# Kernel optimization log

Hardware: AMD Instinct MI355X
Metric: run time of the kernel (lower is better)

The kernel has to match this reference:

```python
import jax, jax.numpy as jnp
import numpy as np
from jax import lax

VOCAB = 50257
EMB = 512
HID = 1024
SEQ = 4096
NUM_LAYERS = 2


def _lstm_layer(x_seq, h0, c0, w_ih, w_hh, b_ih, b_hh):
    """Single-layer LSTM over time. x_seq: [T, in], h0/c0: [H].
    PyTorch gate order: i, f, g, o."""
    # Precompute input projections for all timesteps: [T, 4H]
    xg = x_seq @ w_ih.T + (b_ih + b_hh)

    def step(carry, xg_t):
        h, c = carry
        g = xg_t + h @ w_hh.T  # [4H]
        i, f, gg, o = jnp.split(g, 4)
        i = jax.nn.sigmoid(i)
        f = jax.nn.sigmoid(f)
        gg = jnp.tanh(gg)
        o = jax.nn.sigmoid(o)
        c_new = f * c + i * gg
        h_new = o * jnp.tanh(c_new)
        return (h_new, c_new), h_new

    (h_n, c_n), hs = lax.scan(step, (h0, c0), xg)
    return hs, h_n, c_n  # hs: [T, H]


def setup_inputs() -> dict:
    key = jax.random.key(0)
    ks = jax.random.split(key, 12)
    s = 0.02
    inp = {
        "input": jax.random.randint(ks[0], (SEQ,), 0, VOCAB),
        "h0": jnp.zeros((NUM_LAYERS, 1, HID), jnp.float32),
        "c0": jnp.zeros((NUM_LAYERS, 1, HID), jnp.float32),
        "emb": jax.random.normal(ks[1], (VOCAB, EMB), jnp.float32) * s,
        "w_ih0": jax.random.normal(ks[2], (4 * HID, EMB), jnp.float32) * s,
        "w_hh0": jax.random.normal(ks[3], (4 * HID, HID), jnp.float32) * s,
        "b_ih0": jnp.zeros((4 * HID,), jnp.float32),
        "b_hh0": jnp.zeros((4 * HID,), jnp.float32),
        "w_ih1": jax.random.normal(ks[4], (4 * HID, HID), jnp.float32) * s,
        "w_hh1": jax.random.normal(ks[5], (4 * HID, HID), jnp.float32) * s,
        "b_ih1": jnp.zeros((4 * HID,), jnp.float32),
        "b_hh1": jnp.zeros((4 * HID,), jnp.float32),
        "w_out": jax.random.normal(ks[6], (VOCAB, HID), jnp.float32) * s,
        "b_out": jnp.zeros((VOCAB,), jnp.float32),
    }
    return inp


def reference(input, h0, c0, emb, w_ih0, w_hh0, b_ih0, b_hh0,
              w_ih1, w_hh1, b_ih1, b_hh1, w_out, b_out):
    # Embedding gather: [T, EMB] (batch dim of 1 is implicit)
    x = emb[input]
    # Layer 0
    hs0, h_n0, c_n0 = _lstm_layer(x, h0[0, 0], c0[0, 0], w_ih0, w_hh0, b_ih0, b_hh0)
    # Layer 1 consumes layer-0 hidden sequence
    hs1, h_n1, c_n1 = _lstm_layer(hs0, h0[1, 0], c0[1, 0], w_ih1, w_hh1, b_ih1, b_hh1)
    # lstm_out[-1]: [1, H]
    last = hs1[-1][None, :]
    logits = last @ w_out.T + b_out  # [1, VOCAB]
    output = jax.nn.log_softmax(logits, axis=1)
    h_n = jnp.stack([h_n0, h_n1])[:, None, :]  # [2, 1, H]
    c_n = jnp.stack([c_n0, c_n1])[:, None, :]
    return output, h_n, c_n
```

## Files before the change

### kernel.cpp

```cpp
#include <hip/hip_runtime.h>


#define T_SEQ 4096
#define HID   1024
#define EMBD  512
#define VOCAB 50257
#define NBLK  256
#define TPB   512
#define UB    4
#define NSEG0 48
#define NSEG1 64

#define WS_H0T 0
#define WS_H1T 2048
#define WS_H1F 4096
#define WS_LOG 5120
#define WS_LSE 55377

#define OFF_W0 0
#define OFF_W1 49152
#define OFF_V0 114688
#define OFF_V1 117760
#define OFF_GP 121856
#define OFF_B0 122304
#define OFF_B1 122368
#define SMEM_BYTES 122432

typedef __attribute__((ext_vector_type(8))) short short8;
typedef __attribute__((ext_vector_type(4))) float f32x4;
typedef unsigned long long u64;

__device__ __forceinline__ unsigned short f2bf(float f) {
  unsigned int u = __float_as_uint(f);
  u += 0x7FFFu + ((u >> 16) & 1u);
  return (unsigned short)(u >> 16);
}
__device__ __forceinline__ unsigned int pack2bf(float a, float b) {
  return (unsigned int)f2bf(a) | ((unsigned int)f2bf(b) << 16);
}
__device__ __forceinline__ float sigmoidf_(float x) {
  return 1.f / (1.f + __expf(-x));
}
__device__ __forceinline__ float tanhf_(float x) {
  return 1.f - 2.f / (__expf(2.f * x) + 1.f);
}

template<int CNT>
__device__ __forceinline__ void mm_part(const short8* vf, const short8* wf,
                                        int s0, int lane, float* gout) {
  f32x4 a0 = {0.f, 0.f, 0.f, 0.f};
  f32x4 a1 = a0, a2 = a0, a3 = a0;
  const int grp = lane >> 4;
#pragma unroll
  for (int i = 0; i < CNT; ++i) {
    const int seg = s0 + i;
    short8 av = vf[seg * 4 + grp];
    short8 bv = wf[seg * 64 + lane];
    if ((i & 3) == 0)      a0 = __builtin_amdgcn_mfma_f32_16x16x32_bf16(av, bv, a0, 0, 0, 0);
    else if ((i & 3) == 1) a1 = __builtin_amdgcn_mfma_f32_16x16x32_bf16(av, bv, a1, 0, 0, 0);
    else if ((i & 3) == 2) a2 = __builtin_amdgcn_mfma_f32_16x16x32_bf16(av, bv, a2, 0, 0, 0);
    else                   a3 = __builtin_amdgcn_mfma_f32_16x16x32_bf16(av, bv, a3, 0, 0, 0);
  }
  f32x4 s = (a0 + a1) + (a2 + a3);
  if (lane < 16) gout[lane] = s[0];
}

__global__ __launch_bounds__(TPB, 1) void reset_kernel(
    const float* __restrict__ h0in, unsigned int* __restrict__ ws) {
  const int tid = threadIdx.x;
  u64* H0T = reinterpret_cast<u64*>(ws + WS_H0T);
  u64* H1T = reinterpret_cast<u64*>(ws + WS_H1T);
  H0T[tid] = (u64)pack2bf(h0in[2 * tid], h0in[2 * tid + 1]);
  H1T[tid] = (u64)pack2bf(h0in[HID + 2 * tid], h0in[HID + 2 * tid + 1]);
}

__global__ __launch_bounds__(TPB, 1) void scan_kernel(
    const int* __restrict__ tok,
    const float* __restrict__ h0in, const float* __restrict__ c0in,
    const float* __restrict__ emb,
    const float* __restrict__ wih0, const float* __restrict__ whh0,
    const float* __restrict__ bih0, const float* __restrict__ bhh0,
    const float* __restrict__ wih1, const float* __restrict__ whh1,
    const float* __restrict__ bih1, const float* __restrict__ bhh1,
    float* __restrict__ dout, unsigned int* __restrict__ ws) {
  extern __shared__ char smem[];
  short8* W0f = reinterpret_cast<short8*>(smem + OFF_W0);
  short8* W1f = reinterpret_cast<short8*>(smem + OFF_W1);
  unsigned int* v0w = reinterpret_cast<unsigned int*>(smem + OFF_V0);
  unsigned int* v1w = reinterpret_cast<unsigned int*>(smem + OFF_V1);
  const short8* v0f = reinterpret_cast<const short8*>(smem + OFF_V0);
  const short8* v1f = reinterpret_cast<const short8*>(smem + OFF_V1);
  float* gp  = reinterpret_cast<float*>(smem + OFF_GP);
  float* bs0 = reinterpret_cast<float*>(smem + OFF_B0);
  float* bs1 = reinterpret_cast<float*>(smem + OFF_B1);

  const int tid = threadIdx.x;
  const int bid = blockIdx.x;
  const int lane = tid & 63;
  const int w = tid >> 6;

  for (int slot = tid; slot < NSEG0 * 64; slot += TPB) {
    const int seg = slot >> 6, l = slot & 63;
    const int col = l & 15, grp = l >> 4;
    const int grow = (col >> 2) * HID + bid * UB + (col & 3);
    const int k0 = seg * 32 + grp * 8;
    const float* src = (k0 < EMBD) ? (wih0 + (size_t)grow * EMBD + k0)
                                   : (whh0 + (size_t)grow * HID + (k0 - EMBD));
    const float4* s4 = reinterpret_cast<const float4*>(src);
    float4 f0 = s4[0], f1 = s4[1];
    short8 pk;
    pk[0] = (short)f2bf(f0.x); pk[1] = (short)f2bf(f0.y);
    pk[2] = (short)f2bf(f0.z); pk[3] = (short)f2bf(f0.w);
    pk[4] = (short)f2bf(f1.x); pk[5] = (short)f2bf(f1.y);
    pk[6] = (short)f2bf(f1.z); pk[7] = (short)f2bf(f1.w);
    W0f[slot] = pk;
  }
  for (int slot = tid; slot < NSEG1 * 64; slot += TPB) {
    const int seg = slot >> 6, l = slot & 63;
    const int col = l & 15, grp = l >> 4;
    const int grow = (col >> 2) * HID + bid * UB + (col & 3);
    const int k0 = seg * 32 + grp * 8;
    const float* src = (k0 < HID) ? (wih1 + (size_t)grow * HID + k0)
                                  : (whh1 + (size_t)grow * HID + (k0 - HID));
    const float4* s4 = reinterpret_cast<const float4*>(src);
    float4 f0 = s4[0], f1 = s4[1];
    short8 pk;
    pk[0] = (short)f2bf(f0.x); pk[1] = (short)f2bf(f0.y);
    pk[2] = (short)f2bf(f0.z); pk[3] = (short)f2bf(f0.w);
    pk[4] = (short)f2bf(f1.x); pk[5] = (short)f2bf(f1.y);
    pk[6] = (short)f2bf(f1.z); pk[7] = (short)f2bf(f1.w);
    W1f[slot] = pk;
  }
  if (tid < 16) {
    const int grow = (tid >> 2) * HID + bid * UB + (tid & 3);
    bs0[tid] = bih0[grow] + bhh0[grow];
  } else if (tid < 32) {
    const int c = tid - 16;
    const int grow = (c >> 2) * HID + bid * UB + (c & 3);
    bs1[c] = bih1[grow] + bhh1[grow];
  }

  float cst = 0.f;
  if (w == 0 && lane < UB) cst = c0in[bid * UB + lane];
  if (w == 3 && lane < UB) cst = c0in[HID + bid * UB + lane];

  float xa = 0.f, xb = 0.f;
  if (tid < 256) {
    const float* xp = emb + (size_t)tok[0] * EMBD + tid * 2;
    xa = xp[0]; xb = xp[1];
  }

  u64* H0T = reinterpret_cast<u64*>(ws + WS_H0T);
  u64* H1T = reinterpret_cast<u64*>(ws + WS_H1T);

  for (int r = 1; r <= T_SEQ + 1; ++r) {
    if (tid < 256) {
      v0w[tid] = pack2bf(xa, xb);
      const int ridx = (r < T_SEQ) ? r : (T_SEQ - 1);
      const float* xp = emb + (size_t)tok[ridx] * EMBD + tid * 2;
      xa = xp[0]; xb = xp[1];
    }

    {
      const int p0 = (r - 1) & 1;
      const int p1 = r & 1;
      const unsigned int tg0 = (unsigned int)(r - 1);
      const unsigned int tg1 = (unsigned int)(r - 2);
      const bool need1 = (r >= 2);
      u64 w0 = 0, w1 = 0;
      bool ok0 = false, ok1 = !need1;
      do {
        if (!ok0) {
          w0 = __hip_atomic_load(&H0T[p0 * 512 + tid], __ATOMIC_RELAXED,
                                 __HIP_MEMORY_SCOPE_AGENT);
          ok0 = ((unsigned int)(w0 >> 32) == tg0);
        }
        if (!ok1) {
          w1 = __hip_atomic_load(&H1T[p1 * 512 + tid], __ATOMIC_RELAXED,
                                 __HIP_MEMORY_SCOPE_AGENT);
          ok1 = ((unsigned int)(w1 >> 32) == tg1);
        }
      } while (!(ok0 && ok1));
      const unsigned int d0 = (unsigned int)w0;
      v0w[256 + tid] = d0;
      v1w[tid] = d0;
      if (need1) v1w[512 + tid] = (unsigned int)w1;
    }
    __syncthreads();

    if (w < 3) {
      if (r <= T_SEQ) mm_part<16>(v0f, W0f, w * 16, lane, gp + w * 16);
    } else if (w < 7) {
      if (r >= 2) mm_part<16>(v1f, W1f, (w - 3) * 16, lane, gp + w * 16);
    }
    __syncthreads();

    if (w == 0 && r <= T_SEQ) {
      float hv = 0.f;
      if (lane < UB) {
        const int u = lane;
        float gi = bs0[u], gf = bs0[4 + u], gg = bs0[8 + u], go = bs0[12 + u];
#pragma unroll
        for (int p = 0; p < 3; ++p) {
          gi += gp[p * 16 + u];      gf += gp[p * 16 + 4 + u];
          gg += gp[p * 16 + 8 + u];  go += gp[p * 16 + 12 + u];
        }
        const float c = sigmoidf_(gf) * cst + sigmoidf_(gi) * tanhf_(gg);
        cst = c;
        hv = sigmoidf_(go) * tanhf_(c);
        if (r == T_SEQ) {
          dout[VOCAB + bid * UB + u] = hv;
          dout[VOCAB + 2 * HID + bid * UB + u] = cst;
        }
      }
      const float a = __shfl(hv, 2 * (lane & 1));
      const float b = __shfl(hv, 2 * (lane & 1) + 1);
      if (lane < 2) {
        const u64 word = ((u64)(unsigned int)r << 32) | (u64)pack2bf(a, b);
        __hip_atomic_store(&H0T[(r & 1) * 512 + bid * 2 + lane], word,
                           __ATOMIC_RELAXED, __HIP_MEMORY_SCOPE_AGENT);
      }
    }
    if (w == 3 && r >= 2) {
      float hv = 0.f;
      if (lane < UB) {
        const int u = lane;
        float gi = bs1[u], gf = bs1[4 + u], gg = bs1[8 + u], go = bs1[12 + u];
#pragma unroll
        for (int p = 3; p < 7; ++p) {
          gi += gp[p * 16 + u];      gf += gp[p * 16 + 4 + u];
          gg += gp[p * 16 + 8 + u];  go += gp[p * 16 + 12 + u];
        }
        const float c = sigmoidf_(gf) * cst + sigmoidf_(gi) * tanhf_(gg);
        cst = c;
        hv = sigmoidf_(go) * tanhf_(c);
        if (r - 1 == T_SEQ) {
          float* h1f = reinterpret_cast<float*>(ws + WS_H1F);
          h1f[bid * UB + u] = hv;
          dout[VOCAB + HID + bid * UB + u] = hv;
          dout[VOCAB + 3 * HID + bid * UB + u] = cst;
        }
      }
      const float a = __shfl(hv, 2 * (lane & 1));
      const float b = __shfl(hv, 2 * (lane & 1) + 1);
      if (lane < 2) {
        const u64 word = ((u64)(unsigned int)(r - 1) << 32) | (u64)pack2bf(a, b);
        __hip_atomic_store(&H1T[((r - 1) & 1) * 512 + bid * 2 + lane], word,
                           __ATOMIC_RELAXED, __HIP_MEMORY_SCOPE_AGENT);
      }
    }
  }
}

__global__ __launch_bounds__(256) void logits_kernel(
    const float* __restrict__ wout, const float* __restrict__ bout,
    unsigned int* __restrict__ ws) {
  const float* h1f = reinterpret_cast<const float*>(ws + WS_H1F);
  float* lg = reinterpret_cast<float*>(ws + WS_LOG);
  const int lane = threadIdx.x & 63;
  const int wv = threadIdx.x >> 6;
  const int gw = blockIdx.x * 4 + wv;
  const float4* h4 = reinterpret_cast<const float4*>(h1f);
  float4 h[4];
#pragma unroll
  for (int j = 0; j < 4; ++j) h[j] = h4[j * 64 + lane];
  for (int v = gw; v < VOCAB; v += 1024) {
    const float4* wr = reinterpret_cast<const float4*>(wout + (size_t)v * HID);
    float s = 0.f;
#pragma unroll
    for (int j = 0; j < 4; ++j) {
      float4 x = wr[j * 64 + lane];
      s += x.x * h[j].x + x.y * h[j].y + x.z * h[j].z + x.w * h[j].w;
    }
#pragma unroll
    for (int m = 32; m >= 1; m >>= 1) s += __shfl_xor(s, m, 64);
    if (lane == 0) lg[v] = s + bout[v];
  }
}

__global__ __launch_bounds__(1024) void lse_kernel(unsigned int* __restrict__ ws) {
  const float* lg = reinterpret_cast<const float*>(ws + WS_LOG);
  __shared__ float wred[16];
  __shared__ float mshare;
  const int tid = threadIdx.x;
  float m = -3.4e38f;
  for (int i = tid; i < VOCAB; i += 1024) m = fmaxf(m, lg[i]);
#pragma unroll
  for (int s = 32; s >= 1; s >>= 1) m = fmaxf(m, __shfl_xor(m, s, 64));
  if ((tid & 63) == 0) wred[tid >> 6] = m;
  __syncthreads();
  if (tid == 0) {
    float mm = wred[0];
    for (int i = 1; i < 16; ++i) mm = fmaxf(mm, wred[i]);
    mshare = mm;
  }
  __syncthreads();
  const float M = mshare;
  float a = 0.f;
  for (int i = tid; i < VOCAB; i += 1024) a += __expf(lg[i] - M);
#pragma unroll
  for (int s = 32; s >= 1; s >>= 1) a += __shfl_xor(a, s, 64);
  __syncthreads();
  if ((tid & 63) == 0) wred[tid >> 6] = a;
  __syncthreads();
  if (tid == 0) {
    float ss = 0.f;
    for (int i = 0; i < 16; ++i) ss += wred[i];
    reinterpret_cast<float*>(ws + WS_LSE)[0] = M + logf(ss);
  }
}

__global__ __launch_bounds__(256) void out_kernel(
    const unsigned int* __restrict__ ws, float* __restrict__ dout) {
  const float lse = reinterpret_cast<const float*>(ws + WS_LSE)[0];
  const float* lg = reinterpret_cast<const float*>(ws + WS_LOG);
  const int i = blockIdx.x * 256 + threadIdx.x;
  if (i < VOCAB) dout[i] = lg[i] - lse;
}

extern "C" void kernel_launch(void* const* d_in, const int* in_sizes, int n_in,
                              void* d_out, int out_size, void* d_ws, size_t ws_size,
                              hipStream_t stream) {
  const int*   tok  = (const int*)d_in[0];
  const float* h0in = (const float*)d_in[1];
  const float* c0in = (const float*)d_in[2];
  const float* emb  = (const float*)d_in[3];
  const float* wih0 = (const float*)d_in[4];
  const float* whh0 = (const float*)d_in[5];
  const float* bih0 = (const float*)d_in[6];
  const float* bhh0 = (const float*)d_in[7];
  const float* wih1 = (const float*)d_in[8];
  const float* whh1 = (const float*)d_in[9];
  const float* bih1 = (const float*)d_in[10];
  const float* bhh1 = (const float*)d_in[11];
  const float* wout = (const float*)d_in[12];
  const float* bout = (const float*)d_in[13];
  float* out = (float*)d_out;
  unsigned int* ws = (unsigned int*)d_ws;

  (void)in_sizes; (void)n_in; (void)out_size; (void)ws_size;

  (void)hipFuncSetAttribute((const void*)scan_kernel,
                            hipFuncAttributeMaxDynamicSharedMemorySize, SMEM_BYTES);

  reset_kernel<<<1, TPB, 0, stream>>>(h0in, ws);
  scan_kernel<<<NBLK, TPB, SMEM_BYTES, stream>>>(
      tok, h0in, c0in, emb, wih0, whh0, bih0, bhh0,
      wih1, whh1, bih1, bhh1, out, ws);
  logits_kernel<<<256, 256, 0, stream>>>(wout, bout, ws);
  lse_kernel<<<1, 1024, 0, stream>>>(ws);
  out_kernel<<<(VOCAB + 255) / 256, 256, 0, stream>>>(ws, out);
}
```

Measured before the change: 12.72 ms.

## Cache weight fragments in registers and split hidden-state polling across half-blocks

Each wave now loads its 16 bf16 weight fragments from LDS into registers once before the time loop, so the per-step matmul only reads the activation vector from LDS. Hidden-state exchange switches from 8-byte relaxed atomics to 16-byte coherent (sc0 sc1) inline-asm loads and stores that each carry two tagged words. Threads 0-255 poll layer-0 state and threads 256-511 poll layer-1 state in parallel, instead of every thread polling both. The reset kernel also pre-tags the second buffer slot. The aim is to shorten the per-step sync and LDS latency on the serial critical path, at the cost of higher register pressure and reliance on hand-written cache-control asm and on 16-byte store atomicity.

```diff
diff --git a/kernel.cpp b/kernel.cpp
--- a/kernel.cpp
+++ b/kernel.cpp
@@ -28,6 +28,7 @@
 
 typedef __attribute__((ext_vector_type(8))) short short8;
 typedef __attribute__((ext_vector_type(4))) float f32x4;
+typedef __attribute__((ext_vector_type(4))) unsigned int u32x4;
 typedef unsigned long long u64;
 
 __device__ __forceinline__ unsigned short f2bf(float f) {
@@ -45,21 +46,28 @@
   return 1.f - 2.f / (__expf(2.f * x) + 1.f);
 }
 
-template<int CNT>
-__device__ __forceinline__ void mm_part(const short8* vf, const short8* wf,
-                                        int s0, int lane, float* gout) {
+__device__ __forceinline__ u32x4 load16_cohere(const void* p) {
+  u32x4 r;
+  asm volatile("global_load_dwordx4 %0, %1, off sc0 sc1\n\ts_waitcnt vmcnt(0)"
+               : "=v"(r) : "v"((u64)p) : "memory");
+  return r;
+}
+__device__ __forceinline__ void store16_cohere(void* p, u32x4 v) {
+  asm volatile("global_store_dwordx4 %0, %1, off sc0 sc1"
+               :: "v"((u64)p), "v"(v) : "memory");
+}
+
+__device__ __forceinline__ void mmv(const short8* vf, const short8 (&wr)[16],
+                                    int s0, int grp, float* gout, int lane) {
   f32x4 a0 = {0.f, 0.f, 0.f, 0.f};
   f32x4 a1 = a0, a2 = a0, a3 = a0;
-  const int grp = lane >> 4;
-#pragma unroll
-  for (int i = 0; i < CNT; ++i) {
-    const int seg = s0 + i;
-    short8 av = vf[seg * 4 + grp];
-    short8 bv = wf[seg * 64 + lane];
-    if ((i & 3) == 0)      a0 = __builtin_amdgcn_mfma_f32_16x16x32_bf16(av, bv, a0, 0, 0, 0);
-    else if ((i & 3) == 1) a1 = __builtin_amdgcn_mfma_f32_16x16x32_bf16(av, bv, a1, 0, 0, 0);
-    else if ((i & 3) == 2) a2 = __builtin_amdgcn_mfma_f32_16x16x32_bf16(av, bv, a2, 0, 0, 0);
-    else                   a3 = __builtin_amdgcn_mfma_f32_16x16x32_bf16(av, bv, a3, 0, 0, 0);
+#pragma unroll
+  for (int i = 0; i < 16; ++i) {
+    short8 av = vf[(s0 + i) * 4 + grp];
+    if ((i & 3) == 0)      a0 = __builtin_amdgcn_mfma_f32_16x16x32_bf16(av, wr[i], a0, 0, 0, 0);
+    else if ((i & 3) == 1) a1 = __builtin_amdgcn_mfma_f32_16x16x32_bf16(av, wr[i], a1, 0, 0, 0);
+    else if ((i & 3) == 2) a2 = __builtin_amdgcn_mfma_f32_16x16x32_bf16(av, wr[i], a2, 0, 0, 0);
+    else                   a3 = __builtin_amdgcn_mfma_f32_16x16x32_bf16(av, wr[i], a3, 0, 0, 0);
   }
   f32x4 s = (a0 + a1) + (a2 + a3);
   if (lane < 16) gout[lane] = s[0];
@@ -72,6 +80,8 @@
   u64* H1T = reinterpret_cast<u64*>(ws + WS_H1T);
   H0T[tid] = (u64)pack2bf(h0in[2 * tid], h0in[2 * tid + 1]);
   H1T[tid] = (u64)pack2bf(h0in[HID + 2 * tid], h0in[HID + 2 * tid + 1]);
+  H0T[512 + tid] = 0xFFFFFFFF00000000ULL;
+  H1T[512 + tid] = 0xFFFFFFFF00000000ULL;
 }
 
 __global__ __launch_bounds__(TPB, 1) void scan_kernel(
@@ -98,12 +108,13 @@
   const int bid = blockIdx.x;
   const int lane = tid & 63;
   const int w = tid >> 6;
+  const int grp = lane >> 4;
 
   for (int slot = tid; slot < NSEG0 * 64; slot += TPB) {
     const int seg = slot >> 6, l = slot & 63;
-    const int col = l & 15, grp = l >> 4;
+    const int col = l & 15, g = l >> 4;
     const int grow = (col >> 2) * HID + bid * UB + (col & 3);
-    const int k0 = seg * 32 + grp * 8;
+    const int k0 = seg * 32 + g * 8;
     const float* src = (k0 < EMBD) ? (wih0 + (size_t)grow * EMBD + k0)
                                    : (whh0 + (size_t)grow * HID + (k0 - EMBD));
     const float4* s4 = reinterpret_cast<const float4*>(src);
@@ -117,9 +128,9 @@
   }
   for (int slot = tid; slot < NSEG1 * 64; slot += TPB) {
     const int seg = slot >> 6, l = slot & 63;
-    const int col = l & 15, grp = l >> 4;
+    const int col = l & 15, g = l >> 4;
     const int grow = (col >> 2) * HID + bid * UB + (col & 3);
-    const int k0 = seg * 32 + grp * 8;
+    const int k0 = seg * 32 + g * 8;
     const float* src = (k0 < HID) ? (wih1 + (size_t)grow * HID + k0)
                                   : (whh1 + (size_t)grow * HID + (k0 - HID));
     const float4* s4 = reinterpret_cast<const float4*>(src);
@@ -139,6 +150,17 @@
     const int grow = (c >> 2) * HID + bid * UB + (c & 3);
     bs1[c] = bih1[grow] + bhh1[grow];
   }
+  __syncthreads();
+
+  short8 wr[16];
+  {
+    const short8* wf = (w < 3) ? W0f : W1f;
+    const int s0 = (w < 3) ? w * 16 : (w - 3) * 16;
+    if (w < 7) {
+#pragma unroll
+      for (int i = 0; i < 16; ++i) wr[i] = wf[(s0 + i) * 64 + lane];
+    }
+  }
 
   float cst = 0.f;
   if (w == 0 && lane < UB) cst = c0in[bid * UB + lane];
@@ -161,37 +183,28 @@
       xa = xp[0]; xb = xp[1];
     }
 
-    {
-      const int p0 = (r - 1) & 1;
-      const int p1 = r & 1;
+    if (tid < 256) {
       const unsigned int tg0 = (unsigned int)(r - 1);
+      const u64* src = &H0T[((r - 1) & 1) * 512 + 2 * tid];
+      u32x4 q;
+      do { q = load16_cohere(src); } while (q.y != tg0 || q.w != tg0);
+      const u64 pair = (u64)q.x | ((u64)q.z << 32);
+      *reinterpret_cast<u64*>(&v0w[256 + 2 * tid]) = pair;
+      *reinterpret_cast<u64*>(&v1w[2 * tid]) = pair;
+    } else if (r >= 2) {
+      const int t2 = tid - 256;
       const unsigned int tg1 = (unsigned int)(r - 2);
-      const bool need1 = (r >= 2);
-      u64 w0 = 0, w1 = 0;
-      bool ok0 = false, ok1 = !need1;
-      do {
-        if (!ok0) {
-          w0 = __hip_atomic_load(&H0T[p0 * 512 + tid], __ATOMIC_RELAXED,
-                                 __HIP_MEMORY_SCOPE_AGENT);
-          ok0 = ((unsigned int)(w0 >> 32) == tg0);
-        }
-        if (!ok1) {
-          w1 = __hip_atomic_load(&H1T[p1 * 512 + tid], __ATOMIC_RELAXED,
-                                 __HIP_MEMORY_SCOPE_AGENT);
-          ok1 = ((unsigned int)(w1 >> 32) == tg1);
-        }
-      } while (!(ok0 && ok1));
-      const unsigned int d0 = (unsigned int)w0;
-      v0w[256 + tid] = d0;
-      v1w[tid] = d0;
-      if (need1) v1w[512 + tid] = (unsigned int)w1;
+      const u64* src = &H1T[(r & 1) * 512 + 2 * t2];
+      u32x4 q;
+      do { q = load16_cohere(src); } while (q.y != tg1 || q.w != tg1);
+      *reinterpret_cast<u64*>(&v1w[512 + 2 * t2]) = (u64)q.x | ((u64)q.z << 32);
     }
     __syncthreads();
 
     if (w < 3) {
-      if (r <= T_SEQ) mm_part<16>(v0f, W0f, w * 16, lane, gp + w * 16);
+      if (r <= T_SEQ) mmv(v0f, wr, w * 16, grp, gp + w * 16, lane);
     } else if (w < 7) {
-      if (r >= 2) mm_part<16>(v1f, W1f, (w - 3) * 16, lane, gp + w * 16);
+      if (r >= 2) mmv(v1f, wr, (w - 3) * 16, grp, gp + w * 16, lane);
     }
     __syncthreads();
 
@@ -213,12 +226,13 @@
           dout[VOCAB + 2 * HID + bid * UB + u] = cst;
         }
       }
-      const float a = __shfl(hv, 2 * (lane & 1));
-      const float b = __shfl(hv, 2 * (lane & 1) + 1);
-      if (lane < 2) {
-        const u64 word = ((u64)(unsigned int)r << 32) | (u64)pack2bf(a, b);
-        __hip_atomic_store(&H0T[(r & 1) * 512 + bid * 2 + lane], word,
-                           __ATOMIC_RELAXED, __HIP_MEMORY_SCOPE_AGENT);
+      const float h0v = __shfl(hv, 0), h1v = __shfl(hv, 1);
+      const float h2v = __shfl(hv, 2), h3v = __shfl(hv, 3);
+      if (lane == 0) {
+        u32x4 word;
+        word.x = pack2bf(h0v, h1v); word.y = (unsigned int)r;
+        word.z = pack2bf(h2v, h3v); word.w = (unsigned int)r;
+        store16_cohere(&H0T[(r & 1) * 512 + bid * 2], word);
       }
     }
     if (w == 3 && r >= 2) {
@@ -241,12 +255,13 @@
           dout[VOCAB + 3 * HID + bid * UB + u] = cst;
         }
       }
-      const float a = __shfl(hv, 2 * (lane & 1));
-      const float b = __shfl(hv, 2 * (lane & 1) + 1);
-      if (lane < 2) {
-        const u64 word = ((u64)(unsigned int)(r - 1) << 32) | (u64)pack2bf(a, b);
-        __hip_atomic_store(&H1T[((r - 1) & 1) * 512 + bid * 2 + lane], word,
-                           __ATOMIC_RELAXED, __HIP_MEMORY_SCOPE_AGENT);
+      const float h0v = __shfl(hv, 0), h1v = __shfl(hv, 1);
+      const float h2v = __shfl(hv, 2), h3v = __shfl(hv, 3);
+      if (lane == 0) {
+        u32x4 word;
+        word.x = pack2bf(h0v, h1v); word.y = (unsigned int)(r - 1);
+        word.z = pack2bf(h2v, h3v); word.w = (unsigned int)(r - 1);
+        store16_cohere(&H1T[((r - 1) & 1) * 512 + bid * 2], word);
       }
     }
   }
```

Result: slower. 13.27 ms (+4.4%).

## Replace second block barrier with LDS flag handoff to a dedicated epilogue wave

Applied to the files above, without the earlier changes.

Removes the second __syncthreads per timestep. Each MFMA wave publishes a per-step LDS flag with release semantics, and a dedicated eighth wave spins on those flags with acquire loads before computing the LSTM cell updates for both layers. The input and hidden staging buffers are double-buffered by step parity so the next step's polling can overlap the epilogue. Polling of the global h words is also spread over 448 threads, each issuing three loads per spin. This cuts barrier latency on the serial recurrence path, at the cost of more LDS use, wave spinning, and subtle ordering risk around the buffer reuse.

```diff
diff --git a/kernel.cpp b/kernel.cpp
--- a/kernel.cpp
+++ b/kernel.cpp
@@ -7,6 +7,7 @@
 #define VOCAB 50257
 #define NBLK  256
 #define TPB   512
+#define NPOLL 448
 #define UB    4
 #define NSEG0 48
 #define NSEG1 64
@@ -20,11 +21,12 @@
 #define OFF_W0 0
 #define OFF_W1 49152
 #define OFF_V0 114688
-#define OFF_V1 117760
-#define OFF_GP 121856
-#define OFF_B0 122304
-#define OFF_B1 122368
-#define SMEM_BYTES 122432
+#define OFF_V1 120832
+#define OFF_GP 129024
+#define OFF_B0 129536
+#define OFF_B1 129600
+#define OFF_GF 129664
+#define SMEM_BYTES 129696
 
 typedef __attribute__((ext_vector_type(8))) short short8;
 typedef __attribute__((ext_vector_type(4))) float f32x4;
@@ -44,15 +46,16 @@
 __device__ __forceinline__ float tanhf_(float x) {
   return 1.f - 2.f / (__expf(2.f * x) + 1.f);
 }
-
-template<int CNT>
-__device__ __forceinline__ void mm_part(const short8* vf, const short8* wf,
-                                        int s0, int lane, float* gout) {
+__device__ __forceinline__ unsigned ldsacq(const unsigned* p) {
+  return __hip_atomic_load(p, __ATOMIC_ACQUIRE, __HIP_MEMORY_SCOPE_WORKGROUP);
+}
+
+__device__ __forceinline__ void mmv(const short8* vf, const short8* wf,
+                                    int s0, int grp, float* gout, int lane) {
   f32x4 a0 = {0.f, 0.f, 0.f, 0.f};
   f32x4 a1 = a0, a2 = a0, a3 = a0;
-  const int grp = lane >> 4;
-#pragma unroll
-  for (int i = 0; i < CNT; ++i) {
+#pragma unroll
+  for (int i = 0; i < 16; ++i) {
     const int seg = s0 + i;
     short8 av = vf[seg * 4 + grp];
     short8 bv = wf[seg * 64 + lane];
@@ -70,8 +73,12 @@
   const int tid = threadIdx.x;
   u64* H0T = reinterpret_cast<u64*>(ws + WS_H0T);
   u64* H1T = reinterpret_cast<u64*>(ws + WS_H1T);
-  H0T[tid] = (u64)pack2bf(h0in[2 * tid], h0in[2 * tid + 1]);
-  H1T[tid] = (u64)pack2bf(h0in[HID + 2 * tid], h0in[HID + 2 * tid + 1]);
+  const u64 w0 = (u64)pack2bf(h0in[2 * tid], h0in[2 * tid + 1]);
+  const u64 w1 = (u64)pack2bf(h0in[HID + 2 * tid], h0in[HID + 2 * tid + 1]);
+  __hip_atomic_store(&H0T[tid], w0, __ATOMIC_RELAXED, __HIP_MEMORY_SCOPE_AGENT);
+  __hip_atomic_store(&H1T[tid], w1, __ATOMIC_RELAXED, __HIP_MEMORY_SCOPE_AGENT);
+  __hip_atomic_store(&H0T[512 + tid], 0xFFFFFFFF00000000ULL, __ATOMIC_RELAXED, __HIP_MEMORY_SCOPE_AGENT);
+  __hip_atomic_store(&H1T[512 + tid], 0xFFFFFFFF00000000ULL, __ATOMIC_RELAXED, __HIP_MEMORY_SCOPE_AGENT);
 }
 
 __global__ __launch_bounds__(TPB, 1) void scan_kernel(
@@ -93,17 +100,19 @@
   float* gp  = reinterpret_cast<float*>(smem + OFF_GP);
   float* bs0 = reinterpret_cast<float*>(smem + OFF_B0);
   float* bs1 = reinterpret_cast<float*>(smem + OFF_B1);
+  unsigned* gpflag = reinterpret_cast<unsigned*>(smem + OFF_GF);
 
   const int tid = threadIdx.x;
   const int bid = blockIdx.x;
   const int lane = tid & 63;
   const int w = tid >> 6;
+  const int grp = lane >> 4;
 
   for (int slot = tid; slot < NSEG0 * 64; slot += TPB) {
     const int seg = slot >> 6, l = slot & 63;
-    const int col = l & 15, grp = l >> 4;
+    const int col = l & 15, g = l >> 4;
     const int grow = (col >> 2) * HID + bid * UB + (col & 3);
-    const int k0 = seg * 32 + grp * 8;
+    const int k0 = seg * 32 + g * 8;
     const float* src = (k0 < EMBD) ? (wih0 + (size_t)grow * EMBD + k0)
                                    : (whh0 + (size_t)grow * HID + (k0 - EMBD));
     const float4* s4 = reinterpret_cast<const float4*>(src);
@@ -117,9 +126,9 @@
   }
   for (int slot = tid; slot < NSEG1 * 64; slot += TPB) {
     const int seg = slot >> 6, l = slot & 63;
-    const int col = l & 15, grp = l >> 4;
+    const int col = l & 15, g = l >> 4;
     const int grow = (col >> 2) * HID + bid * UB + (col & 3);
-    const int k0 = seg * 32 + grp * 8;
+    const int k0 = seg * 32 + g * 8;
     const float* src = (k0 < HID) ? (wih1 + (size_t)grow * HID + k0)
                                   : (whh1 + (size_t)grow * HID + (k0 - HID));
     const float4* s4 = reinterpret_cast<const float4*>(src);
@@ -139,10 +148,13 @@
     const int grow = (c >> 2) * HID + bid * UB + (c & 3);
     bs1[c] = bih1[grow] + bhh1[grow];
   }
+  if (tid < 8) gpflag[tid] = 0u;
 
   float cst = 0.f;
-  if (w == 0 && lane < UB) cst = c0in[bid * UB + lane];
-  if (w == 3 && lane < UB) cst = c0in[HID + bid * UB + lane];
+  if (w == 7) {
+    if (lane < UB) cst = c0in[bid * UB + lane];
+    else if (lane >= 8 && lane < 8 + UB) cst = c0in[HID + bid * UB + (lane - 8)];
+  }
 
   float xa = 0.f, xb = 0.f;
   if (tid < 256) {
@@ -153,100 +165,138 @@
   u64* H0T = reinterpret_cast<u64*>(ws + WS_H0T);
   u64* H1T = reinterpret_cast<u64*>(ws + WS_H1T);
 
+  __syncthreads();
+
   for (int r = 1; r <= T_SEQ + 1; ++r) {
-    if (tid < 256) {
-      v0w[tid] = pack2bf(xa, xb);
-      const int ridx = (r < T_SEQ) ? r : (T_SEQ - 1);
-      const float* xp = emb + (size_t)tok[ridx] * EMBD + tid * 2;
-      xa = xp[0]; xb = xp[1];
-    }
-
-    {
+    const int pb = r & 1;
+
+    if (tid < NPOLL) {
+      if (tid < 256) {
+        v0w[pb * 768 + tid] = pack2bf(xa, xb);
+        const int ridx = (r < T_SEQ) ? r : (T_SEQ - 1);
+        const float* xp = emb + (size_t)tok[ridx] * EMBD + tid * 2;
+        xa = xp[0]; xb = xp[1];
+      }
+
       const int p0 = (r - 1) & 1;
       const int p1 = r & 1;
-      const unsigned int tg0 = (unsigned int)(r - 1);
-      const unsigned int tg1 = (unsigned int)(r - 2);
-      const bool need1 = (r >= 2);
-      u64 w0 = 0, w1 = 0;
-      bool ok0 = false, ok1 = !need1;
+      const unsigned tgh0 = (unsigned)(r - 1);
+      const unsigned tgh1 = (unsigned)(r - 2);
+      const int i0 = tid;
+      const int i1 = tid + 448;
+      const int i2 = (tid < 128) ? tid + 896 : tid;
+
+      u64* ap0 = &H0T[p0 * 512 + i0]; unsigned tg0 = tgh0;
+      u64 *ap1, *ap2; unsigned tg1, tg2;
+      if (i1 < 512)      { ap1 = &H0T[p0 * 512 + i1]; tg1 = tgh0; }
+      else if (r >= 2)   { ap1 = &H1T[p1 * 512 + (i1 - 512)]; tg1 = tgh1; }
+      else               { ap1 = ap0; tg1 = tg0; }
+      if (i2 < 512)      { ap2 = &H0T[p0 * 512 + i2]; tg2 = tgh0; }
+      else if (r >= 2)   { ap2 = &H1T[p1 * 512 + (i2 - 512)]; tg2 = tgh1; }
+      else               { ap2 = ap0; tg2 = tg0; }
+
+      u64 d0 = 0, d1 = 0, d2 = 0;
+      bool k0 = false, k1 = false, k2 = false;
       do {
-        if (!ok0) {
-          w0 = __hip_atomic_load(&H0T[p0 * 512 + tid], __ATOMIC_RELAXED,
-                                 __HIP_MEMORY_SCOPE_AGENT);
-          ok0 = ((unsigned int)(w0 >> 32) == tg0);
-        }
-        if (!ok1) {
-          w1 = __hip_atomic_load(&H1T[p1 * 512 + tid], __ATOMIC_RELAXED,
-                                 __HIP_MEMORY_SCOPE_AGENT);
-          ok1 = ((unsigned int)(w1 >> 32) == tg1);
-        }
-      } while (!(ok0 && ok1));
-      const unsigned int d0 = (unsigned int)w0;
-      v0w[256 + tid] = d0;
-      v1w[tid] = d0;
-      if (need1) v1w[512 + tid] = (unsigned int)w1;
+        const u64 s0 = __hip_atomic_load(ap0, __ATOMIC_RELAXED, __HIP_MEMORY_SCOPE_AGENT);
+        const u64 s1 = __hip_atomic_load(ap1, __ATOMIC_RELAXED, __HIP_MEMORY_SCOPE_AGENT);
+        const u64 s2 = __hip_atomic_load(ap2, __ATOMIC_RELAXED, __HIP_MEMORY_SCOPE_AGENT);
+        if (!k0 && (unsigned)(s0 >> 32) == tg0) { d0 = s0; k0 = true; }
+        if (!k1 && (unsigned)(s1 >> 32) == tg1) { d1 = s1; k1 = true; }
+        if (!k2 && (unsigned)(s2 >> 32) == tg2) { d2 = s2; k2 = true; }
+      } while (!(k0 && k1 && k2));
+
+      {
+        const unsigned lo = (unsigned)d0;
+        v0w[pb * 768 + 256 + i0] = lo;
+        v1w[pb * 1024 + i0] = lo;
+      }
+      if (i1 < 512) {
+        const unsigned lo = (unsigned)d1;
+        v0w[pb * 768 + 256 + i1] = lo;
+        v1w[pb * 1024 + i1] = lo;
+      } else if (r >= 2) {
+        v1w[pb * 1024 + 512 + (i1 - 512)] = (unsigned)d1;
+      }
+      if (tid < 128 && r >= 2) {
+        v1w[pb * 1024 + 512 + (i2 - 512)] = (unsigned)d2;
+      }
     }
     __syncthreads();
 
     if (w < 3) {
-      if (r <= T_SEQ) mm_part<16>(v0f, W0f, w * 16, lane, gp + w * 16);
+      if (r <= T_SEQ) {
+        mmv(v0f + pb * 192, W0f, w * 16, grp, gp + w * 16, lane);
+        if (lane == 0)
+          __hip_atomic_store(&gpflag[w], (unsigned)r, __ATOMIC_RELEASE,
+                             __HIP_MEMORY_SCOPE_WORKGROUP);
+      }
     } else if (w < 7) {
-      if (r >= 2) mm_part<16>(v1f, W1f, (w - 3) * 16, lane, gp + w * 16);
-    }
-    __syncthreads();
-
-    if (w == 0 && r <= T_SEQ) {
-      float hv = 0.f;
-      if (lane < UB) {
-        const int u = lane;
-        float gi = bs0[u], gf = bs0[4 + u], gg = bs0[8 + u], go = bs0[12 + u];
-#pragma unroll
-        for (int p = 0; p < 3; ++p) {
-          gi += gp[p * 16 + u];      gf += gp[p * 16 + 4 + u];
-          gg += gp[p * 16 + 8 + u];  go += gp[p * 16 + 12 + u];
+      if (r >= 2) {
+        mmv(v1f + pb * 256, W1f, (w - 3) * 16, grp, gp + w * 16, lane);
+        if (lane == 0)
+          __hip_atomic_store(&gpflag[w], (unsigned)r, __ATOMIC_RELEASE,
+                             __HIP_MEMORY_SCOPE_WORKGROUP);
+      }
+    } else {
+      const unsigned ru = (unsigned)r;
+      if (r <= T_SEQ) {
+        while (ldsacq(&gpflag[0]) < ru || ldsacq(&gpflag[1]) < ru ||
+               ldsacq(&gpflag[2]) < ru) { }
+        float hv = 0.f;
+        if (lane < UB) {
+          const int u = lane;
+          float gi = bs0[u], gf = bs0[4 + u], gg = bs0[8 + u], go = bs0[12 + u];
+#pragma unroll
+          for (int p = 0; p < 3; ++p) {
+            gi += gp[p * 16 + u];      gf += gp[p * 16 + 4 + u];
+            gg += gp[p * 16 + 8 + u];  go += gp[p * 16 + 12 + u];
+          }
+          const float c = sigmoidf_(gf) * cst + sigmoidf_(gi) * tanhf_(gg);
+          cst = c;
+          hv = sigmoidf_(go) * tanhf_(c);
+          if (r == T_SEQ) {
+            dout[VOCAB + bid * UB + u] = hv;
+            dout[VOCAB + 2 * HID + bid * UB + u] = cst;
+          }
         }
-        const float c = sigmoidf_(gf) * cst + sigmoidf_(gi) * tanhf_(gg);
-        cst = c;
-        hv = sigmoidf_(go) * tanhf_(c);
-        if (r == T_SEQ) {
-          dout[VOCAB + bid * UB + u] = hv;
-          dout[VOCAB + 2 * HID + bid * UB + u] = cst;
+        const float a = __shfl(hv, 2 * (lane & 1));
+        const float b = __shfl(hv, 2 * (lane & 1) + 1);
+        if (lane < 2) {
+          const u64 word = ((u64)ru << 32) | (u64)pack2bf(a, b);
+          __hip_atomic_store(&H0T[(r & 1) * 512 + bid * 2 + lane], word,
+                             __ATOMIC_RELAXED, __HIP_MEMORY_SCOPE_AGENT);
         }
       }
-      const float a = __shfl(hv, 2 * (lane & 1));
-      const float b = __shfl(hv, 2 * (lane & 1) + 1);
-      if (lane < 2) {
-        const u64 word = ((u64)(unsigned int)r << 32) | (u64)pack2bf(a, b);
-        __hip_atomic_store(&H0T[(r & 1) * 512 + bid * 2 + lane], word,
-                           __ATOMIC_RELAXED, __HIP_MEMORY_SCOPE_AGENT);
-      }
-    }
-    if (w == 3 && r >= 2) {
-      float hv = 0.f;
-      if (lane < UB) {
-        const int u = lane;
-        float gi = bs1[u], gf = bs1[4 + u], gg = bs1[8 + u], go = bs1[12 + u];
-#pragma unroll
-        for (int p = 3; p < 7; ++p) {
-          gi += gp[p * 16 + u];      gf += gp[p * 16 + 4 + u];
-          gg += gp[p * 16 + 8 + u];  go += gp[p * 16 + 12 + u];
+      if (r >= 2) {
+        while (ldsacq(&gpflag[3]) < ru || ldsacq(&gpflag[4]) < ru ||
+               ldsacq(&gpflag[5]) < ru || ldsacq(&gpflag[6]) < ru) { }
+        float hv = 0.f;
+        if (lane >= 8 && lane < 8 + UB) {
+          const int u = lane - 8;
+          float gi = bs1[u], gf = bs1[4 + u], gg = bs1[8 + u], go = bs1[12 + u];
+#pragma unroll
+          for (int p = 3; p < 7; ++p) {
+            gi += gp[p * 16 + u];      gf += gp[p * 16 + 4 + u];
+            gg += gp[p * 16 + 8 + u];  go += gp[p * 16 + 12 + u];
+          }
+          const float c = sigmoidf_(gf) * cst + sigmoidf_(gi) * tanhf_(gg);
+          cst = c;
+          hv = sigmoidf_(go) * tanhf_(c);
+          if (r - 1 == T_SEQ) {
+            float* h1f = reinterpret_cast<float*>(ws + WS_H1F);
+            h1f[bid * UB + u] = hv;
+            dout[VOCAB + HID + bid * UB + u] = hv;
+            dout[VOCAB + 3 * HID + bid * UB + u] = cst;
+          }
         }
-        const float c = sigmoidf_(gf) * cst + sigmoidf_(gi) * tanhf_(gg);
-        cst = c;
-        hv = sigmoidf_(go) * tanhf_(c);
-        if (r - 1 == T_SEQ) {
-          float* h1f = reinterpret_cast<float*>(ws + WS_H1F);
-          h1f[bid * UB + u] = hv;
-          dout[VOCAB + HID + bid * UB + u] = hv;
-          dout[VOCAB + 3 * HID + bid * UB + u] = cst;
+        const float a = __shfl(hv, 8 + 2 * (lane & 1));
+        const float b = __shfl(hv, 9 + 2 * (lane & 1));
+        if (lane >= 8 && lane < 10) {
+          const u64 word = ((u64)(unsigned)(r - 1) << 32) | (u64)pack2bf(a, b);
+          __hip_atomic_store(&H1T[((r - 1) & 1) * 512 + bid * 2 + (lane - 8)], word,
+                             __ATOMIC_RELAXED, __HIP_MEMORY_SCOPE_AGENT);
         }
-      }
-      const float a = __shfl(hv, 2 * (lane & 1));
-      const float b = __shfl(hv, 2 * (lane & 1) + 1);
-      if (lane < 2) {
-        const u64 word = ((u64)(unsigned int)(r - 1) << 32) | (u64)pack2bf(a, b);
-        __hip_atomic_store(&H1T[((r - 1) & 1) * 512 + bid * 2 + lane], word,
-                           __ATOMIC_RELAXED, __HIP_MEMORY_SCOPE_AGENT);
       }
     }
   }
```

Measured after the change: 19.97 ms. +57.0%, slower.

## Warp-specialize LSTM scan with register-resident weights and LDS flag sync

Applied to the files above, without the earlier changes.

Replaces the block-wide __syncthreads step loop with specialized wavefronts: loader waves poll the global hidden-state tags and fill double-buffered LDS vectors, while compute waves keep their bf16 weight slices in VGPRs and run MFMA. Coordination uses per-wave acquire/release flags in LDS. The point is to drop the two barriers per timestep, overlap the layer-0 and layer-1 polling with compute, and avoid re-reading weights from LDS every step. The cost is much more register pressure (up to 32 f32x4 weight fragments per lane), spin-wait LDS traffic, and a more fragile ordering protocol. The reset kernel also poisons the second parity buffer so stale tags cannot match.

```diff
diff --git a/kernel.cpp b/kernel.cpp
--- a/kernel.cpp
+++ b/kernel.cpp
@@ -8,8 +8,6 @@
 #define NBLK  256
 #define TPB   512
 #define UB    4
-#define NSEG0 48
-#define NSEG1 64
 
 #define WS_H0T 0
 #define WS_H1T 2048
@@ -20,11 +18,22 @@
 #define OFF_W0 0
 #define OFF_W1 49152
 #define OFF_V0 114688
-#define OFF_V1 117760
-#define OFF_GP 121856
-#define OFF_B0 122304
-#define OFF_B1 122368
-#define SMEM_BYTES 122432
+#define OFF_V1 120832
+#define OFF_PP0 124928
+#define OFF_PP1 125056
+#define OFF_B0 125184
+#define OFF_B1 125248
+#define OFF_FL 125312
+#define SMEM_BYTES 125376
+
+#define FL_SF0 0
+#define FL_SF1 1
+#define FL_SF4 4
+#define FL_SF5 5
+#define FL_PA0 8
+#define FL_PA1 9
+#define FL_C3  10
+#define FL_C7  11
 
 typedef __attribute__((ext_vector_type(8))) short short8;
 typedef __attribute__((ext_vector_type(4))) float f32x4;
@@ -44,25 +53,34 @@
 __device__ __forceinline__ float tanhf_(float x) {
   return 1.f - 2.f / (__expf(2.f * x) + 1.f);
 }
-
-template<int CNT>
-__device__ __forceinline__ void mm_part(const short8* vf, const short8* wf,
-                                        int s0, int lane, float* gout) {
+__device__ __forceinline__ unsigned ldsacq(const unsigned* p) {
+  return __hip_atomic_load(p, __ATOMIC_ACQUIRE, __HIP_MEMORY_SCOPE_WORKGROUP);
+}
+__device__ __forceinline__ void ldsrel(unsigned* p, unsigned v) {
+  __hip_atomic_store(p, v, __ATOMIC_RELEASE, __HIP_MEMORY_SCOPE_WORKGROUP);
+}
+__device__ __forceinline__ u64 agld(const u64* p) {
+  return __hip_atomic_load(p, __ATOMIC_RELAXED, __HIP_MEMORY_SCOPE_AGENT);
+}
+__device__ __forceinline__ void agst(u64* p, u64 v) {
+  __hip_atomic_store(p, v, __ATOMIC_RELAXED, __HIP_MEMORY_SCOPE_AGENT);
+}
+
+template<int NS>
+__device__ __forceinline__ f32x4 mm_regs(const f32x4 (&fr)[NS],
+                                         const short8* avb, int grp) {
   f32x4 a0 = {0.f, 0.f, 0.f, 0.f};
   f32x4 a1 = a0, a2 = a0, a3 = a0;
-  const int grp = lane >> 4;
-#pragma unroll
-  for (int i = 0; i < CNT; ++i) {
-    const int seg = s0 + i;
-    short8 av = vf[seg * 4 + grp];
-    short8 bv = wf[seg * 64 + lane];
+#pragma unroll
+  for (int i = 0; i < NS; ++i) {
+    short8 av = avb[i * 4 + grp];
+    short8 bv = __builtin_bit_cast(short8, fr[i]);
     if ((i & 3) == 0)      a0 = __builtin_amdgcn_mfma_f32_16x16x32_bf16(av, bv, a0, 0, 0, 0);
     else if ((i & 3) == 1) a1 = __builtin_amdgcn_mfma_f32_16x16x32_bf16(av, bv, a1, 0, 0, 0);
     else if ((i & 3) == 2) a2 = __builtin_amdgcn_mfma_f32_16x16x32_bf16(av, bv, a2, 0, 0, 0);
     else                   a3 = __builtin_amdgcn_mfma_f32_16x16x32_bf16(av, bv, a3, 0, 0, 0);
   }
-  f32x4 s = (a0 + a1) + (a2 + a3);
-  if (lane < 16) gout[lane] = s[0];
+  return (a0 + a1) + (a2 + a3);
 }
 
 __global__ __launch_bounds__(TPB, 1) void reset_kernel(
@@ -70,8 +88,12 @@
   const int tid = threadIdx.x;
   u64* H0T = reinterpret_cast<u64*>(ws + WS_H0T);
   u64* H1T = reinterpret_cast<u64*>(ws + WS_H1T);
-  H0T[tid] = (u64)pack2bf(h0in[2 * tid], h0in[2 * tid + 1]);
-  H1T[tid] = (u64)pack2bf(h0in[HID + 2 * tid], h0in[HID + 2 * tid + 1]);
+  const u64 w0 = (u64)pack2bf(h0in[2 * tid], h0in[2 * tid + 1]);
+  const u64 w1 = (u64)pack2bf(h0in[HID + 2 * tid], h0in[HID + 2 * tid + 1]);
+  agst(&H0T[tid], w0);
+  agst(&H1T[tid], w1);
+  agst(&H0T[512 + tid], 0xFFFFFFFF00000000ULL);
+  agst(&H1T[512 + tid], 0xFFFFFFFF00000000ULL);
 }
 
 __global__ __launch_bounds__(TPB, 1) void scan_kernel(
@@ -90,20 +112,23 @@
   unsigned int* v1w = reinterpret_cast<unsigned int*>(smem + OFF_V1);
   const short8* v0f = reinterpret_cast<const short8*>(smem + OFF_V0);
   const short8* v1f = reinterpret_cast<const short8*>(smem + OFF_V1);
-  float* gp  = reinterpret_cast<float*>(smem + OFF_GP);
+  float* pp0 = reinterpret_cast<float*>(smem + OFF_PP0);
+  float* pp1 = reinterpret_cast<float*>(smem + OFF_PP1);
   float* bs0 = reinterpret_cast<float*>(smem + OFF_B0);
   float* bs1 = reinterpret_cast<float*>(smem + OFF_B1);
+  unsigned* flg = reinterpret_cast<unsigned*>(smem + OFF_FL);
 
   const int tid = threadIdx.x;
   const int bid = blockIdx.x;
   const int lane = tid & 63;
   const int w = tid >> 6;
-
-  for (int slot = tid; slot < NSEG0 * 64; slot += TPB) {
+  const int grp = lane >> 4;
+
+  for (int slot = tid; slot < 48 * 64; slot += TPB) {
     const int seg = slot >> 6, l = slot & 63;
-    const int col = l & 15, grp = l >> 4;
+    const int col = l & 15, g = l >> 4;
     const int grow = (col >> 2) * HID + bid * UB + (col & 3);
-    const int k0 = seg * 32 + grp * 8;
+    const int k0 = seg * 32 + g * 8;
     const float* src = (k0 < EMBD) ? (wih0 + (size_t)grow * EMBD + k0)
                                    : (whh0 + (size_t)grow * HID + (k0 - EMBD));
     const float4* s4 = reinterpret_cast<const float4*>(src);
@@ -115,11 +140,11 @@
     pk[6] = (short)f2bf(f1.z); pk[7] = (short)f2bf(f1.w);
     W0f[slot] = pk;
   }
-  for (int slot = tid; slot < NSEG1 * 64; slot += TPB) {
+  for (int slot = tid; slot < 64 * 64; slot += TPB) {
     const int seg = slot >> 6, l = slot & 63;
-    const int col = l & 15, grp = l >> 4;
+    const int col = l & 15, g = l >> 4;
     const int grow = (col >> 2) * HID + bid * UB + (col & 3);
-    const int k0 = seg * 32 + grp * 8;
+    const int k0 = seg * 32 + g * 8;
     const float* src = (k0 < HID) ? (wih1 + (size_t)grow * HID + k0)
                                   : (whh1 + (size_t)grow * HID + (k0 - HID));
     const float4* s4 = reinterpret_cast<const float4*>(src);
@@ -139,115 +164,168 @@
     const int grow = (c >> 2) * HID + bid * UB + (c & 3);
     bs1[c] = bih1[grow] + bhh1[grow];
   }
-
-  float cst = 0.f;
-  if (w == 0 && lane < UB) cst = c0in[bid * UB + lane];
-  if (w == 3 && lane < UB) cst = c0in[HID + bid * UB + lane];
-
-  float xa = 0.f, xb = 0.f;
-  if (tid < 256) {
-    const float* xp = emb + (size_t)tok[0] * EMBD + tid * 2;
-    xa = xp[0]; xb = xp[1];
-  }
+  if (tid < 16) flg[tid] = 0u;
 
   u64* H0T = reinterpret_cast<u64*>(ws + WS_H0T);
   u64* H1T = reinterpret_cast<u64*>(ws + WS_H1T);
 
-  for (int r = 1; r <= T_SEQ + 1; ++r) {
-    if (tid < 256) {
-      v0w[tid] = pack2bf(xa, xb);
+  __syncthreads();
+
+  if (w < 2) {
+    const int t = tid;
+    const float4* emb4 = reinterpret_cast<const float4*>(emb);
+    float4 xcur = emb4[(size_t)tok[0] * 128 + t];
+    for (int r = 1; r <= T_SEQ + 1; ++r) {
+      const int p = r & 1;
       const int ridx = (r < T_SEQ) ? r : (T_SEQ - 1);
-      const float* xp = emb + (size_t)tok[ridx] * EMBD + tid * 2;
-      xa = xp[0]; xb = xp[1];
-    }
-
-    {
-      const int p0 = (r - 1) & 1;
-      const int p1 = r & 1;
-      const unsigned int tg0 = (unsigned int)(r - 1);
-      const unsigned int tg1 = (unsigned int)(r - 2);
-      const bool need1 = (r >= 2);
-      u64 w0 = 0, w1 = 0;
-      bool ok0 = false, ok1 = !need1;
+      float4 xnext = emb4[(size_t)tok[ridx] * 128 + t];
+      if (r >= 3) {
+        const unsigned need = (unsigned)(r - 2);
+        while (ldsacq(&flg[FL_C3]) < need || ldsacq(&flg[FL_PA1]) < need ||
+               ldsacq(&flg[FL_C7]) < need) { }
+      }
+      v0w[p * 768 + 2 * t]     = pack2bf(xcur.x, xcur.y);
+      v0w[p * 768 + 2 * t + 1] = pack2bf(xcur.z, xcur.w);
+      const unsigned tg = (unsigned)(r - 1);
+      u64* ap = &H0T[((r - 1) & 1) * 512 + 4 * t];
+      u64 d0 = 0, d1 = 0, d2 = 0, d3 = 0;
+      bool k0 = false, k1 = false, k2 = false, k3 = false;
       do {
-        if (!ok0) {
-          w0 = __hip_atomic_load(&H0T[p0 * 512 + tid], __ATOMIC_RELAXED,
-                                 __HIP_MEMORY_SCOPE_AGENT);
-          ok0 = ((unsigned int)(w0 >> 32) == tg0);
-        }
-        if (!ok1) {
-          w1 = __hip_atomic_load(&H1T[p1 * 512 + tid], __ATOMIC_RELAXED,
-                                 __HIP_MEMORY_SCOPE_AGENT);
-          ok1 = ((unsigned int)(w1 >> 32) == tg1);
-        }
-      } while (!(ok0 && ok1));
-      const unsigned int d0 = (unsigned int)w0;
-      v0w[256 + tid] = d0;
-      v1w[tid] = d0;
-      if (need1) v1w[512 + tid] = (unsigned int)w1;
-    }
-    __syncthreads();
-
-    if (w < 3) {
-      if (r <= T_SEQ) mm_part<16>(v0f, W0f, w * 16, lane, gp + w * 16);
-    } else if (w < 7) {
-      if (r >= 2) mm_part<16>(v1f, W1f, (w - 3) * 16, lane, gp + w * 16);
-    }
-    __syncthreads();
-
-    if (w == 0 && r <= T_SEQ) {
+        if (!k0) { d0 = agld(ap + 0); k0 = ((unsigned)(d0 >> 32) == tg); }
+        if (!k1) { d1 = agld(ap + 1); k1 = ((unsigned)(d1 >> 32) == tg); }
+        if (!k2) { d2 = agld(ap + 2); k2 = ((unsigned)(d2 >> 32) == tg); }
+        if (!k3) { d3 = agld(ap + 3); k3 = ((unsigned)(d3 >> 32) == tg); }
+      } while (!(k0 && k1 && k2 && k3));
+      unsigned* dst = &v0w[p * 768 + 256 + 4 * t];
+      dst[0] = (unsigned)d0; dst[1] = (unsigned)d1;
+      dst[2] = (unsigned)d2; dst[3] = (unsigned)d3;
+      ldsrel(&flg[w], (unsigned)r);
+      xcur = xnext;
+    }
+  } else if (w == 2) {
+    f32x4 fr[24];
+    const f32x4* Wr = reinterpret_cast<const f32x4*>(W0f);
+#pragma unroll
+    for (int i = 0; i < 24; ++i) fr[i] = Wr[i * 64 + lane];
+#pragma unroll
+    for (int i = 0; i < 24; ++i) asm volatile("" : "+v"(fr[i]));
+    for (int r = 1; r <= T_SEQ; ++r) {
+      const int p = r & 1;
+      const unsigned ru = (unsigned)r;
+      while (ldsacq(&flg[FL_SF0]) < ru || ldsacq(&flg[FL_SF1]) < ru) { }
+      f32x4 s = mm_regs<24>(fr, v0f + p * 192, grp);
+      if (lane < 16) pp0[p * 16 + lane] = s[0];
+      ldsrel(&flg[FL_PA0], ru);
+    }
+  } else if (w == 3) {
+    f32x4 fr[24];
+    const f32x4* Wr = reinterpret_cast<const f32x4*>(W0f);
+#pragma unroll
+    for (int i = 0; i < 24; ++i) fr[i] = Wr[(24 + i) * 64 + lane];
+#pragma unroll
+    for (int i = 0; i < 24; ++i) asm volatile("" : "+v"(fr[i]));
+    float cst = (lane < UB) ? c0in[bid * UB + lane] : 0.f;
+    for (int r = 1; r <= T_SEQ; ++r) {
+      const int p = r & 1;
+      const unsigned ru = (unsigned)r;
+      while (ldsacq(&flg[FL_SF0]) < ru || ldsacq(&flg[FL_SF1]) < ru) { }
+      f32x4 s = mm_regs<24>(fr, v0f + p * 192 + 96, grp);
+      ldsrel(&flg[FL_C3], ru);
+      while (ldsacq(&flg[FL_PA0]) < ru) { }
+      float g = 0.f;
+      if (lane < 16) g = s[0] + pp0[p * 16 + lane] + bs0[lane];
+      const int u = lane & 3;
+      const float gi = __shfl(g, u),      gf = __shfl(g, 4 + u);
+      const float gg = __shfl(g, 8 + u),  go = __shfl(g, 12 + u);
       float hv = 0.f;
       if (lane < UB) {
-        const int u = lane;
-        float gi = bs0[u], gf = bs0[4 + u], gg = bs0[8 + u], go = bs0[12 + u];
-#pragma unroll
-        for (int p = 0; p < 3; ++p) {
-          gi += gp[p * 16 + u];      gf += gp[p * 16 + 4 + u];
-          gg += gp[p * 16 + 8 + u];  go += gp[p * 16 + 12 + u];
-        }
         const float c = sigmoidf_(gf) * cst + sigmoidf_(gi) * tanhf_(gg);
         cst = c;
         hv = sigmoidf_(go) * tanhf_(c);
         if (r == T_SEQ) {
-          dout[VOCAB + bid * UB + u] = hv;
-          dout[VOCAB + 2 * HID + bid * UB + u] = cst;
+          dout[VOCAB + bid * UB + lane] = hv;
+          dout[VOCAB + 2 * HID + bid * UB + lane] = c;
         }
       }
       const float a = __shfl(hv, 2 * (lane & 1));
       const float b = __shfl(hv, 2 * (lane & 1) + 1);
-      if (lane < 2) {
-        const u64 word = ((u64)(unsigned int)r << 32) | (u64)pack2bf(a, b);
-        __hip_atomic_store(&H0T[(r & 1) * 512 + bid * 2 + lane], word,
-                           __ATOMIC_RELAXED, __HIP_MEMORY_SCOPE_AGENT);
-      }
-    }
-    if (w == 3 && r >= 2) {
+      if (lane < 2)
+        agst(&H0T[(r & 1) * 512 + bid * 2 + lane],
+             ((u64)ru << 32) | (u64)pack2bf(a, b));
+    }
+  } else if (w < 6) {
+    const int t = tid - 256;
+    for (int r = 2; r <= T_SEQ + 1; ++r) {
+      const int p = r & 1;
+      const unsigned tg = (unsigned)(r - 2);
+      u64* ap = &H1T[p * 512 + 4 * t];
+      u64 d0 = 0, d1 = 0, d2 = 0, d3 = 0;
+      bool k0 = false, k1 = false, k2 = false, k3 = false;
+      do {
+        if (!k0) { d0 = agld(ap + 0); k0 = ((unsigned)(d0 >> 32) == tg); }
+        if (!k1) { d1 = agld(ap + 1); k1 = ((unsigned)(d1 >> 32) == tg); }
+        if (!k2) { d2 = agld(ap + 2); k2 = ((unsigned)(d2 >> 32) == tg); }
+        if (!k3) { d3 = agld(ap + 3); k3 = ((unsigned)(d3 >> 32) == tg); }
+      } while (!(k0 && k1 && k2 && k3));
+      unsigned* dst = &v1w[p * 512 + 4 * t];
+      dst[0] = (unsigned)d0; dst[1] = (unsigned)d1;
+      dst[2] = (unsigned)d2; dst[3] = (unsigned)d3;
+      ldsrel(&flg[w], (unsigned)r);
+    }
+  } else if (w == 6) {
+    f32x4 fr[32];
+    const f32x4* Wr = reinterpret_cast<const f32x4*>(W1f);
+#pragma unroll
+    for (int i = 0; i < 32; ++i) fr[i] = Wr[i * 64 + lane];
+#pragma unroll
+    for (int i = 0; i < 32; ++i) asm volatile("" : "+v"(fr[i]));
+    for (int r = 2; r <= T_SEQ + 1; ++r) {
+      const int p = r & 1;
+      const unsigned ru = (unsigned)r;
+      while (ldsacq(&flg[FL_SF0]) < ru || ldsacq(&flg[FL_SF1]) < ru ||
+             ldsacq(&flg[FL_SF4]) < ru || ldsacq(&flg[FL_SF5]) < ru) { }
+      f32x4 s = mm_regs<32>(fr, v0f + p * 192 + 64, grp);
+      if (lane < 16) pp1[p * 16 + lane] = s[0];
+      ldsrel(&flg[FL_PA1], ru);
+    }
+  } else {
+    f32x4 fr[32];
+    const f32x4* Wr = reinterpret_cast<const f32x4*>(W1f);
+#pragma unroll
+    for (int i = 0; i < 32; ++i) fr[i] = Wr[(32 + i) * 64 + lane];
+#pragma unroll
+    for (int i = 0; i < 32; ++i) asm volatile("" : "+v"(fr[i]));
+    float cst = (lane < UB) ? c0in[HID + bid * UB + lane] : 0.f;
+    for (int r = 2; r <= T_SEQ + 1; ++r) {
+      const int p = r & 1;
+      const unsigned ru = (unsigned)r;
+      while (ldsacq(&flg[FL_SF0]) < ru || ldsacq(&flg[FL_SF1]) < ru ||
+             ldsacq(&flg[FL_SF4]) < ru || ldsacq(&flg[FL_SF5]) < ru) { }
+      f32x4 s = mm_regs<32>(fr, v1f + p * 128, grp);
+      ldsrel(&flg[FL_C7], ru);
+      while (ldsacq(&flg[FL_PA1]) < ru) { }
+      float g = 0.f;
+      if (lane < 16) g = s[0] + pp1[p * 16 + lane] + bs1[lane];
+      const int u = lane & 3;
+      const float gi = __shfl(g, u),      gf = __shfl(g, 4 + u);
+      const float gg = __shfl(g, 8 + u),  go = __shfl(g, 12 + u);
       float hv = 0.f;
       if (lane < UB) {
-        const int u = lane;
-        float gi = bs1[u], gf = bs1[4 + u], gg = bs1[8 + u], go = bs1[12 + u];
-#pragma unroll
-        for (int p = 3; p < 7; ++p) {
-          gi += gp[p * 16 + u];      gf += gp[p * 16 + 4 + u];
-          gg += gp[p * 16 + 8 + u];  go += gp[p * 16 + 12 + u];
-        }
         const float c = sigmoidf_(gf) * cst + sigmoidf_(gi) * tanhf_(gg);
         cst = c;
         hv = sigmoidf_(go) * tanhf_(c);
-        if (r - 1 == T_SEQ) {
+        if (r == T_SEQ + 1) {
           float* h1f = reinterpret_cast<float*>(ws + WS_H1F);
-          h1f[bid * UB + u] = hv;
-          dout[VOCAB + HID + bid * UB + u] = hv;
-          dout[VOCAB + 3 * HID + bid * UB + u] = cst;
+          h1f[bid * UB + lane] = hv;
+          dout[VOCAB + HID + bid * UB + lane] = hv;
+          dout[VOCAB + 3 * HID + bid * UB + lane] = c;
         }
       }
       const float a = __shfl(hv, 2 * (lane & 1));
       const float b = __shfl(hv, 2 * (lane & 1) + 1);
-      if (lane < 2) {
-        const u64 word = ((u64)(unsigned int)(r - 1) << 32) | (u64)pack2bf(a, b);
-        __hip_atomic_store(&H1T[((r - 1) & 1) * 512 + bid * 2 + lane], word,
-                           __ATOMIC_RELAXED, __HIP_MEMORY_SCOPE_AGENT);
-      }
+      if (lane < 2)
+        agst(&H1T[((r - 1) & 1) * 512 + bid * 2 + lane],
+             ((u64)(unsigned)(r - 1) << 32) | (u64)pack2bf(a, b));
     }
   }
 }
```

Result: slower. 16.76 ms (+31.8%).
